# Optimization experiments

Measured on AMD Instinct MI355X. Metric: run time of the kernel, lower is better.

## Reference

```python
import jax, jax.numpy as jnp
import numpy as np

# MxCorrelation (MXNet/FlowNet correlation) parameters
PAD = 4            # pad_size
K = 1              # kernel_size
MAXD = 4           # max_displacement
S1 = 1             # stride1 (output stride)
S2 = 1             # stride2 (displacement stride)


def setup_inputs() -> dict:
    key = jax.random.key(0)
    k1, k2 = jax.random.split(key)
    B, C, H, W = 8, 128, 128, 128
    input1 = jax.random.normal(k1, (B, C, H, W), dtype=jnp.float32)
    input2 = jax.random.normal(k2, (B, C, H, W), dtype=jnp.float32)
    return {"input1": input1, "input2": input2}


def _correlation(a, b):
    # a, b: [B, C, H, W]; returns [B, gw*gw, top_h, top_w]
    B, C, H, W = a.shape
    kr = (K - 1) // 2                       # kernel radius
    border = MAXD + kr                      # border in padded coords
    pa = jnp.pad(a, ((0, 0), (0, 0), (PAD, PAD), (PAD, PAD)))
    pb = jnp.pad(b, ((0, 0), (0, 0), (PAD, PAD), (PAD, PAD)))
    Hp, Wp = H + 2 * PAD, W + 2 * PAD
    th = -(-(Hp - 2 * border) // S1)        # top_height (ceil div)
    tw = -(-(Wp - 2 * border) // S1)        # top_width
    ngr = MAXD // S2                        # neighborhood grid radius
    gw = 2 * ngr + 1                        # grid width -> gw*gw out channels
    sumelems = jnp.float32(K * K * C)       # MXNet normalization

    out = []
    # channel order matches MXNet: row displacement p outer, col q inner
    for p in range(-ngr, ngr + 1):
        for q in range(-ngr, ngr + 1):
            s2p, s2q = p * S2, q * S2
            acc = jnp.zeros((B, th, tw), dtype=a.dtype)
            for dy in range(-kr, kr + 1):
                for dx in range(-kr, kr + 1):
                    A = pa[:, :, border + dy: border + dy + th * S1: S1,
                           border + dx: border + dx + tw * S1: S1]
                    Bm = pb[:, :, border + s2p + dy: border + s2p + dy + th * S1: S1,
                            border + s2q + dx: border + s2q + dx + tw * S1: S1]
                    acc = acc + jnp.sum(A * Bm, axis=1)  # reduce over channels
            out.append(acc / sumelems)
    return jnp.stack(out, axis=1)  # [B, gw*gw, th, tw]


def reference(input1, input2):
    return _correlation(input1, input2)
```

## Files before the change

kernel.cpp:

```cpp
#include <hip/hip_runtime.h>


typedef __fp16 h2 __attribute__((ext_vector_type(2)));

#define BW2 144

#if __has_builtin(__builtin_amdgcn_fdot2)
  #define FDOT2(a, b, c) __builtin_amdgcn_fdot2((a), (b), (c), false)
#else
  static __device__ inline float FDOT2(h2 a, h2 b, float c) {
      return c + (float)a.x * (float)b.x + (float)a.y * (float)b.y;
  }
#endif

static __device__ inline float pk2f(float lo, float hi) {
    h2 v = __builtin_amdgcn_cvt_pkrtz(lo, hi);
    return __builtin_bit_cast(float, v);
}
static __device__ inline h2 f2h2(float f) { return __builtin_bit_cast(h2, f); }

__global__ __launch_bounds__(576, 5)
void corr_kernel(const float* __restrict__ A, const float* __restrict__ B,
                 float* __restrict__ out)
{
    const int bidx = blockIdx.x;
    const int bb = bidx & 7;
    const int y  = bidx >> 3;

    const int tid  = threadIdx.x;
    const int wave = tid >> 6;
    const int lane = tid & 63;
    const int cs   = lane >> 5;
    const int x0   = (lane & 31) << 2;

    __shared__ h2 a_s[2][2][128];
    __shared__ h2 b_s[2][9][2][BW2];

    {
        float4* p = (float4*)&b_s[0][0][0][0];
        const int total = 2 * 9 * 2 * BW2 / 4;
        for (int i = tid; i < total; i += 576) p[i] = make_float4(0.f, 0.f, 0.f, 0.f);
    }

    float acc[9][4];
    #pragma unroll
    for (int q = 0; q < 9; ++q)
        #pragma unroll
        for (int i = 0; i < 4; ++i) acc[q][i] = 0.f;

    const long plane = 128L * 128L;
    const float* Abase = A + (long)bb * 128 * plane + (long)y * 128;
    const float* Bbase = B + (long)bb * 128 * plane;

    const int br  = tid >> 5;
    const int bi4 = (tid & 31) << 2;
    const int bpr = br >> 1;
    const int bpp = br & 1;
    const int bys = y + bpr - 4;
    const bool bval = ((unsigned)bys < 128u) && (br < 18);
    const float* Bsrc = Bbase + (long)bys * 128 + bi4;

    const bool aact = tid < 64;
    const int app = (tid >> 5) & 1;
    const int ai4 = (tid & 31) << 2;

    float4 rb0 = make_float4(0.f,0.f,0.f,0.f), rb1 = rb0, ra0 = rb0, ra1 = rb0;

    auto load_chunk = [&](int ch0) {
        if (bval) {
            const int c0 = ch0 + (bpp << 1);
            rb0 = *(const float4*)(Bsrc + (long)c0 * plane);
            rb1 = *(const float4*)(Bsrc + (long)(c0 + 1) * plane);
        }
        if (aact) {
            const int c0 = ch0 + (app << 1);
            ra0 = *(const float4*)(Abase + (long)c0 * plane + ai4);
            ra1 = *(const float4*)(Abase + (long)(c0 + 1) * plane + ai4);
        }
    };
    auto write_stage = [&](int buf) {
        if (bval) {
            float4 w;
            w.x = pk2f(rb0.x, rb1.x);
            w.y = pk2f(rb0.y, rb1.y);
            w.z = pk2f(rb0.z, rb1.z);
            w.w = pk2f(rb0.w, rb1.w);
            *(float4*)&b_s[buf][bpr][bpp][4 + bi4] = w;
        }
        if (aact) {
            float4 w;
            w.x = pk2f(ra0.x, ra1.x);
            w.y = pk2f(ra0.y, ra1.y);
            w.z = pk2f(ra0.z, ra1.z);
            w.w = pk2f(ra0.w, ra1.w);
            *(float4*)&a_s[buf][app][ai4] = w;
        }
    };

    load_chunk(0);
    __syncthreads();
    write_stage(0);
    load_chunk(4);
    __syncthreads();

    for (int k = 0; k < 32; ++k) {
        const int buf = k & 1;
        if (k + 1 < 32) write_stage(buf ^ 1);
        if (k + 2 < 32) load_chunk((k + 2) << 2);
        {
            const float4 av = *(const float4*)&a_s[buf][cs][x0];
            const float4 b0 = *(const float4*)&b_s[buf][wave][cs][x0];
            const float4 b1 = *(const float4*)&b_s[buf][wave][cs][x0 + 4];
            const float4 b2 = *(const float4*)&b_s[buf][wave][cs][x0 + 8];
            const h2 a2[4] = { f2h2(av.x), f2h2(av.y), f2h2(av.z), f2h2(av.w) };
            const h2 w[12] = { f2h2(b0.x), f2h2(b0.y), f2h2(b0.z), f2h2(b0.w),
                               f2h2(b1.x), f2h2(b1.y), f2h2(b1.z), f2h2(b1.w),
                               f2h2(b2.x), f2h2(b2.y), f2h2(b2.z), f2h2(b2.w) };
            #pragma unroll
            for (int q = 0; q < 9; ++q)
                #pragma unroll
                for (int i = 0; i < 4; ++i)
                    acc[q][i] = FDOT2(a2[i], w[q + i], acc[q][i]);
        }
        __syncthreads();
    }

    #pragma unroll
    for (int q = 0; q < 9; ++q)
        #pragma unroll
        for (int i = 0; i < 4; ++i)
            acc[q][i] += __shfl_down(acc[q][i], 32);

    if (cs == 0) {
        const float scale = 1.0f / 128.0f;
        float* obase = out + (((long)bb * 81 + (long)wave * 9) * 128 + y) * 128 + x0;
        #pragma unroll
        for (int q = 0; q < 9; ++q) {
            const float4 v = make_float4(acc[q][0] * scale, acc[q][1] * scale,
                                         acc[q][2] * scale, acc[q][3] * scale);
            *(float4*)(obase + (long)q * plane) = v;
        }
    }
}

extern "C" void kernel_launch(void* const* d_in, const int* in_sizes, int n_in,
                              void* d_out, int out_size, void* d_ws, size_t ws_size,
                              hipStream_t stream) {
    const float* a = (const float*)d_in[0];
    const float* b = (const float*)d_in[1];
    float* out = (float*)d_out;
    hipLaunchKernelGGL(corr_kernel, dim3(1024), dim3(576), 0, stream, a, b, out);
}
```

Before: 233.0 us.

## Split row displacements across three blocks per output row

Each output row is now handled by three 192-thread blocks, one per group of three row displacements, instead of one 576-thread block covering all nine. This triples the grid size and shrinks shared memory per block, which should improve occupancy and scheduling granularity. In exchange, the A row is loaded three times and the per-block load of the B tile is smaller, so total global traffic for A rises.

```diff
diff --git a/kernel.cpp b/kernel.cpp
--- a/kernel.cpp
+++ b/kernel.cpp
@@ -19,27 +19,33 @@
 }
 static __device__ inline h2 f2h2(float f) { return __builtin_bit_cast(h2, f); }
 
-__global__ __launch_bounds__(576, 5)
+__global__ __launch_bounds__(192, 4)
 void corr_kernel(const float* __restrict__ A, const float* __restrict__ B,
                  float* __restrict__ out)
 {
     const int bidx = blockIdx.x;
     const int bb = bidx & 7;
-    const int y  = bidx >> 3;
+    const int t2 = bidx >> 3;
+    const int y  = t2 & 127;
+    const int pg = t2 >> 7;
 
     const int tid  = threadIdx.x;
     const int wave = tid >> 6;
     const int lane = tid & 63;
     const int cs   = lane >> 5;
     const int x0   = (lane & 31) << 2;
+    const int pr   = pg * 3 + wave;
 
     __shared__ h2 a_s[2][2][128];
-    __shared__ h2 b_s[2][9][2][BW2];
+    __shared__ h2 b_s[2][3][2][BW2];
 
     {
-        float4* p = (float4*)&b_s[0][0][0][0];
-        const int total = 2 * 9 * 2 * BW2 / 4;
-        for (int i = tid; i < total; i += 576) p[i] = make_float4(0.f, 0.f, 0.f, 0.f);
+        float4* p = (float4*)&a_s[0][0][0];
+        const int na = 2 * 2 * 128 / 4;
+        for (int i = tid; i < na; i += 192) p[i] = make_float4(0.f, 0.f, 0.f, 0.f);
+        float4* pb = (float4*)&b_s[0][0][0][0];
+        const int nb = 2 * 3 * 2 * BW2 / 4;
+        for (int i = tid; i < nb; i += 192) pb[i] = make_float4(0.f, 0.f, 0.f, 0.f);
     }
 
     float acc[9][4];
@@ -52,17 +58,16 @@
     const float* Abase = A + (long)bb * 128 * plane + (long)y * 128;
     const float* Bbase = B + (long)bb * 128 * plane;
 
-    const int br  = tid >> 5;
-    const int bi4 = (tid & 31) << 2;
-    const int bpr = br >> 1;
-    const int bpp = br & 1;
-    const int bys = y + bpr - 4;
-    const bool bval = ((unsigned)bys < 128u) && (br < 18);
-    const float* Bsrc = Bbase + (long)bys * 128 + bi4;
+    const int i4  = (tid & 31) << 2;
+    const int rp  = tid >> 5;
+    const int brw = rp >> 1;
+    const int bpp = rp & 1;
+    const int bys = y + pg * 3 + brw - 4;
+    const bool bval = (unsigned)bys < 128u;
+    const float* Bsrc = Bbase + (long)bys * 128 + i4;
 
     const bool aact = tid < 64;
     const int app = (tid >> 5) & 1;
-    const int ai4 = (tid & 31) << 2;
 
     float4 rb0 = make_float4(0.f,0.f,0.f,0.f), rb1 = rb0, ra0 = rb0, ra1 = rb0;
 
@@ -74,8 +79,8 @@
         }
         if (aact) {
             const int c0 = ch0 + (app << 1);
-            ra0 = *(const float4*)(Abase + (long)c0 * plane + ai4);
-            ra1 = *(const float4*)(Abase + (long)(c0 + 1) * plane + ai4);
+            ra0 = *(const float4*)(Abase + (long)c0 * plane + i4);
+            ra1 = *(const float4*)(Abase + (long)(c0 + 1) * plane + i4);
         }
     };
     auto write_stage = [&](int buf) {
@@ -85,7 +90,7 @@
             w.y = pk2f(rb0.y, rb1.y);
             w.z = pk2f(rb0.z, rb1.z);
             w.w = pk2f(rb0.w, rb1.w);
-            *(float4*)&b_s[buf][bpr][bpp][4 + bi4] = w;
+            *(float4*)&b_s[buf][brw][bpp][4 + i4] = w;
         }
         if (aact) {
             float4 w;
@@ -93,7 +98,7 @@
             w.y = pk2f(ra0.y, ra1.y);
             w.z = pk2f(ra0.z, ra1.z);
             w.w = pk2f(ra0.w, ra1.w);
-            *(float4*)&a_s[buf][app][ai4] = w;
+            *(float4*)&a_s[buf][app][i4] = w;
         }
     };
 
@@ -133,7 +138,7 @@
 
     if (cs == 0) {
         const float scale = 1.0f / 128.0f;
-        float* obase = out + (((long)bb * 81 + (long)wave * 9) * 128 + y) * 128 + x0;
+        float* obase = out + (((long)bb * 81 + (long)pr * 9) * 128 + y) * 128 + x0;
         #pragma unroll
         for (int q = 0; q < 9; ++q) {
             const float4 v = make_float4(acc[q][0] * scale, acc[q][1] * scale,
@@ -149,5 +154,5 @@
     const float* a = (const float*)d_in[0];
     const float* b = (const float*)d_in[1];
     float* out = (float*)d_out;
-    hipLaunchKernelGGL(corr_kernel, dim3(1024), dim3(576), 0, stream, a, b, out);
+    hipLaunchKernelGGL(corr_kernel, dim3(3072), dim3(192), 0, stream, a, b, out);
 }
```

Result: faster. 197.5 us (-15.2%).

## Retile correlation blocks to two output rows by three displacement rows

Applied to the files above, without the earlier changes.

Each block now computes two output rows for three row-displacements (6 waves, 384 threads) rather than one output row for all nine displacements. B rows staged per block drop from 9 to 4, shared between the two output rows, and all threads take part in the global-to-LDS loads. The launch goes from 1024 to 1536 blocks, with smaller LDS use and more resident blocks per CU. In exchange, B rows are re-read across the three displacement groups and A rows are loaded once per group.

```diff
diff --git a/kernel.cpp b/kernel.cpp
--- a/kernel.cpp
+++ b/kernel.cpp
@@ -19,27 +19,34 @@
 }
 static __device__ inline h2 f2h2(float f) { return __builtin_bit_cast(h2, f); }
 
-__global__ __launch_bounds__(576, 5)
+__global__ __launch_bounds__(384, 7)
 void corr_kernel(const float* __restrict__ A, const float* __restrict__ B,
                  float* __restrict__ out)
 {
     const int bidx = blockIdx.x;
-    const int bb = bidx & 7;
-    const int y  = bidx >> 3;
+    const int bb   = bidx & 7;
+    const int rest = bidx >> 3;
+    const int ygrp = rest & 63;
+    const int pgrp = rest >> 6;
+    const int y0   = ygrp << 1;
 
     const int tid  = threadIdx.x;
-    const int wave = tid >> 6;
+    const int wv   = tid >> 6;
     const int lane = tid & 63;
     const int cs   = lane >> 5;
     const int x0   = (lane & 31) << 2;
+    const int ylw  = wv & 1;
+    const int pl   = wv >> 1;
+    const int slot = ylw + pl;
+    const int pr   = pgrp * 3 + pl;
 
-    __shared__ h2 a_s[2][2][128];
-    __shared__ h2 b_s[2][9][2][BW2];
+    __shared__ h2 a_s[2][2][2][128];
+    __shared__ h2 b_s[2][4][2][BW2];
 
     {
-        float4* p = (float4*)&b_s[0][0][0][0];
-        const int total = 2 * 9 * 2 * BW2 / 4;
-        for (int i = tid; i < total; i += 576) p[i] = make_float4(0.f, 0.f, 0.f, 0.f);
+        float4* pb = (float4*)&b_s[0][0][0][0];
+        const int nb = 2 * 4 * 2 * BW2 / 4;
+        for (int i = tid; i < nb; i += 384) pb[i] = make_float4(0.f, 0.f, 0.f, 0.f);
     }
 
     float acc[9][4];
@@ -49,51 +56,51 @@
         for (int i = 0; i < 4; ++i) acc[q][i] = 0.f;
 
     const long plane = 128L * 128L;
-    const float* Abase = A + (long)bb * 128 * plane + (long)y * 128;
-    const float* Bbase = B + (long)bb * 128 * plane;
+    const float* Abat = A + (long)bb * 128 * plane;
+    const float* Bbat = B + (long)bb * 128 * plane;
 
-    const int br  = tid >> 5;
-    const int bi4 = (tid & 31) << 2;
-    const int bpr = br >> 1;
-    const int bpp = br & 1;
-    const int bys = y + bpr - 4;
-    const bool bval = ((unsigned)bys < 128u) && (br < 18);
-    const float* Bsrc = Bbase + (long)bys * 128 + bi4;
+    const bool brole = tid < 256;
+    const float* gsrc;
+    int gpair;
+    bool gvalid;
+    h2* wptr0; h2* wptr1;
+    if (brole) {
+        const int col = tid & 31;
+        gpair = (tid >> 5) & 1;
+        const int sl = tid >> 6;
+        const int ys = y0 + pgrp * 3 - 4 + sl;
+        gvalid = (unsigned)ys < 128u;
+        gsrc = Bbat + (long)ys * 128 + (col << 2);
+        wptr0 = &b_s[0][sl][gpair][4 + (col << 2)];
+        wptr1 = &b_s[1][sl][gpair][4 + (col << 2)];
+    } else {
+        const int u = tid - 256;
+        const int col = u & 31;
+        gpair = (u >> 5) & 1;
+        const int yl = u >> 6;
+        gvalid = true;
+        gsrc = Abat + (long)(y0 + yl) * 128 + (col << 2);
+        wptr0 = &a_s[0][yl][gpair][col << 2];
+        wptr1 = &a_s[1][yl][gpair][col << 2];
+    }
 
-    const bool aact = tid < 64;
-    const int app = (tid >> 5) & 1;
-    const int ai4 = (tid & 31) << 2;
-
-    float4 rb0 = make_float4(0.f,0.f,0.f,0.f), rb1 = rb0, ra0 = rb0, ra1 = rb0;
+    float4 r0 = make_float4(0.f, 0.f, 0.f, 0.f), r1 = r0;
 
     auto load_chunk = [&](int ch0) {
-        if (bval) {
-            const int c0 = ch0 + (bpp << 1);
-            rb0 = *(const float4*)(Bsrc + (long)c0 * plane);
-            rb1 = *(const float4*)(Bsrc + (long)(c0 + 1) * plane);
-        }
-        if (aact) {
-            const int c0 = ch0 + (app << 1);
-            ra0 = *(const float4*)(Abase + (long)c0 * plane + ai4);
-            ra1 = *(const float4*)(Abase + (long)(c0 + 1) * plane + ai4);
+        if (gvalid) {
+            const long off = (long)(ch0 + (gpair << 1)) * plane;
+            r0 = *(const float4*)(gsrc + off);
+            r1 = *(const float4*)(gsrc + off + plane);
         }
     };
     auto write_stage = [&](int buf) {
-        if (bval) {
+        if (gvalid) {
             float4 w;
-            w.x = pk2f(rb0.x, rb1.x);
-            w.y = pk2f(rb0.y, rb1.y);
-            w.z = pk2f(rb0.z, rb1.z);
-            w.w = pk2f(rb0.w, rb1.w);
-            *(float4*)&b_s[buf][bpr][bpp][4 + bi4] = w;
-        }
-        if (aact) {
-            float4 w;
-            w.x = pk2f(ra0.x, ra1.x);
-            w.y = pk2f(ra0.y, ra1.y);
-            w.z = pk2f(ra0.z, ra1.z);
-            w.w = pk2f(ra0.w, ra1.w);
-            *(float4*)&a_s[buf][app][ai4] = w;
+            w.x = pk2f(r0.x, r1.x);
+            w.y = pk2f(r0.y, r1.y);
+            w.z = pk2f(r0.z, r1.z);
+            w.w = pk2f(r0.w, r1.w);
+            *(float4*)(buf ? wptr1 : wptr0) = w;
         }
     };
 
@@ -108,10 +115,10 @@
         if (k + 1 < 32) write_stage(buf ^ 1);
         if (k + 2 < 32) load_chunk((k + 2) << 2);
         {
-            const float4 av = *(const float4*)&a_s[buf][cs][x0];
-            const float4 b0 = *(const float4*)&b_s[buf][wave][cs][x0];
-            const float4 b1 = *(const float4*)&b_s[buf][wave][cs][x0 + 4];
-            const float4 b2 = *(const float4*)&b_s[buf][wave][cs][x0 + 8];
+            const float4 av = *(const float4*)&a_s[buf][ylw][cs][x0];
+            const float4 b0 = *(const float4*)&b_s[buf][slot][cs][x0];
+            const float4 b1 = *(const float4*)&b_s[buf][slot][cs][x0 + 4];
+            const float4 b2 = *(const float4*)&b_s[buf][slot][cs][x0 + 8];
             const h2 a2[4] = { f2h2(av.x), f2h2(av.y), f2h2(av.z), f2h2(av.w) };
             const h2 w[12] = { f2h2(b0.x), f2h2(b0.y), f2h2(b0.z), f2h2(b0.w),
                                f2h2(b1.x), f2h2(b1.y), f2h2(b1.z), f2h2(b1.w),
@@ -133,7 +140,8 @@
 
     if (cs == 0) {
         const float scale = 1.0f / 128.0f;
-        float* obase = out + (((long)bb * 81 + (long)wave * 9) * 128 + y) * 128 + x0;
+        const int y = y0 + ylw;
+        float* obase = out + (((long)bb * 81 + (long)pr * 9) * 128 + y) * 128 + x0;
         #pragma unroll
         for (int q = 0; q < 9; ++q) {
             const float4 v = make_float4(acc[q][0] * scale, acc[q][1] * scale,
@@ -149,5 +157,5 @@
     const float* a = (const float*)d_in[0];
     const float* b = (const float*)d_in[1];
     float* out = (float*)d_out;
-    hipLaunchKernelGGL(corr_kernel, dim3(1024), dim3(576), 0, stream, a, b, out);
+    hipLaunchKernelGGL(corr_kernel, dim3(1536), dim3(384), 0, stream, a, b, out);
 }
```

Result: faster. 203.8 us (-12.5%).
